# Optimization experiments

Measured on AMD Instinct MI355X. Metric: run time of the kernel, lower is better.

Reference implementation:

```python
import jax, jax.numpy as jnp
import numpy as np
from jax import lax

EPS = 1e-08
PAD = 1  # kernel_size // 2 for k=3


def setup_inputs() -> dict:
    key = jax.random.key(0)
    k1, k2, k3, k4 = jax.random.split(key, 4)
    B, Cin, Cout, H, W, K, S = 16, 256, 256, 64, 64, 3, 512
    x = jax.random.normal(k1, (B, Cin, H, W), dtype=jnp.float32)
    style = jax.random.normal(k2, (B, S), dtype=jnp.float32)
    mod_weight = jax.random.normal(k3, (Cin, S), dtype=jnp.float32)
    mod_bias = jnp.zeros((Cin,), dtype=jnp.float32)
    weight = jax.random.normal(k4, (1, Cout, Cin, K, K), dtype=jnp.float32)
    bias = jnp.zeros((1, Cout, 1, 1), dtype=jnp.float32)
    return {"x": x, "style": style, "mod_weight": mod_weight,
            "mod_bias": mod_bias, "weight": weight, "bias": bias}


def reference(x, style, mod_weight, mod_bias, weight, bias):
    # EqualizedLinear modulation (lr_mul = 1.0): s[b, cin]
    s = style @ mod_weight.T + mod_bias  # [B, Cin]
    # per-sample modulated weights: [B, Cout, Cin, K, K]
    w = weight * s[:, None, :, None, None]
    # demodulation: rsqrt of sum over (Cin, K, K)
    demod = lax.rsqrt(jnp.sum(w * w, axis=(2, 3, 4)) + EPS)  # [B, Cout]
    w = w * demod[:, :, None, None, None]

    # per-sample conv2d (groups=B equivalent) via vmap over batch
    def conv_one(xb, wb):
        # xb: [Cin, H, W], wb: [Cout, Cin, K, K]
        return lax.conv_general_dilated(
            xb[None], wb, window_strides=(1, 1),
            padding=[(PAD, PAD), (PAD, PAD)],
            dimension_numbers=("NCHW", "OIHW", "NCHW"))[0]

    out = jax.vmap(conv_one)(x, w)  # [B, Cout, H, W]
    return out + bias
```

## Files before the change

kernel.cpp:

```cpp
#include <hip/hip_runtime.h>

#define EPS 1e-8f
#define THREADS 512

typedef __attribute__((ext_vector_type(8))) short short8;
typedef __attribute__((ext_vector_type(4))) float f32x4;
typedef __attribute__((ext_vector_type(8))) unsigned short u16x8;

static __device__ __forceinline__ unsigned short f2bf(float f) {
  unsigned int u = __float_as_uint(f);
  u += 0x7FFF + ((u >> 16) & 1);
  return (unsigned short)(u >> 16);
}

__global__ void k_prep(const float* __restrict__ style, const float* __restrict__ mw,
                       const float* __restrict__ mb, float* __restrict__ s_out,
                       const float* __restrict__ weight, float* __restrict__ wsq,
                       unsigned short* __restrict__ wbf) {
  __shared__ float sm[2304];
  int t = threadIdx.x;
  if (blockIdx.x < 16) {
    int b = blockIdx.x;
    sm[t]       = style[b*512 + t];
    sm[t + 256] = style[b*512 + 256 + t];
    __syncthreads();
    const float4* row = (const float4*)(mw + (size_t)t*512);
    float acc = 0.f;
#pragma unroll 4
    for (int i = 0; i < 128; ++i) {
      float4 m = row[i];
      acc += m.x*sm[4*i] + m.y*sm[4*i+1] + m.z*sm[4*i+2] + m.w*sm[4*i+3];
    }
    s_out[b*256 + t] = acc + mb[t];
  } else {
    int co = blockIdx.x - 16;
    for (int q = t; q < 576; q += 256)
      *(float4*)&sm[q*4] = *(const float4*)(weight + (size_t)co*2304 + q*4);
    __syncthreads();
    int ci = t;
    int c = ci >> 6, cil = ci & 63;
    int base = ((co*128 + cil*2) ^ ((co & 7) << 4)) >> 1;
    float sum = 0.f;
#pragma unroll
    for (int r = 0; r < 9; ++r) {
      float v = sm[ci*9 + r];
      sum += v*v;
      wbf[(size_t)(c*9 + r)*16384 + base] = f2bf(v);
    }
    wsq[co*256 + ci] = sum;
  }
}

__global__ void k_demod(const float* __restrict__ s, const float* __restrict__ wsq,
                        float* __restrict__ dm) {
  int b = blockIdx.x, t = threadIdx.x;
  __shared__ float s2[256];
  float sv = s[b*256 + t];
  s2[t] = sv*sv;
  __syncthreads();
  const float4* row = (const float4*)(wsq + (size_t)t*256);
  float acc = 0.f;
#pragma unroll 4
  for (int i = 0; i < 64; ++i) {
    float4 q = row[i];
    acc += q.x*s2[4*i] + q.y*s2[4*i+1] + q.z*s2[4*i+2] + q.w*s2[4*i+3];
  }
  dm[b*256 + t] = rsqrtf(acc + EPS);
}

__global__ void k_pad(const float* __restrict__ x, const float* __restrict__ s,
                      unsigned short* __restrict__ xp) {
  int bid = blockIdx.x;
  int b = bid / 66, gh = bid - b*66;
  int t = threadIdx.x;
  size_t rowbase = (size_t)(b*66 + gh) * (66*256);
  u16x8* rp = (u16x8*)(xp + rowbase);
  if (gh == 0 || gh == 65) {
    u16x8 z = (u16x8)0;
    for (int q = t; q < 2112; q += 256) rp[q] = z;
    return;
  }
  int h = gh - 1;
  __shared__ float sl[256];
  __shared__ unsigned short xl[64*256];
  sl[t] = s[b*256 + t];
  __syncthreads();
  int w4 = (t & 15) * 4, o0 = t >> 4;
#pragma unroll
  for (int p = 0; p < 2; ++p) {
    int oct = o0 + p*16;
    u16x8 outv[4];
#pragma unroll
    for (int j = 0; j < 8; ++j) {
      int ci = oct*8 + j;
      float4 v = *(const float4*)(x + ((size_t)(b*256 + ci)*64 + h)*64 + w4);
      float sc = sl[ci];
      outv[0][j] = (short)f2bf(v.x * sc);
      outv[1][j] = (short)f2bf(v.y * sc);
      outv[2][j] = (short)f2bf(v.z * sc);
      outv[3][j] = (short)f2bf(v.w * sc);
    }
#pragma unroll
    for (int k = 0; k < 4; ++k) {
      int w = w4 + k;
      int byte = w*512 + ((oct ^ (w & 31)) << 4);
      *(u16x8*)((char*)xl + byte) = outv[k];
    }
  }
  __syncthreads();
  u16x8 z = (u16x8)0;
  if (t < 32) rp[t] = z;
  else if (t < 64) rp[65*32 + (t - 32)] = z;
  for (int q = t; q < 2048; q += 256) {
    int w2 = q >> 5, slot = q & 31;
    u16x8 v = *(const u16x8*)((char*)xl + w2*512 + ((slot ^ (w2 & 31)) << 4));
    rp[(w2 + 1)*32 + slot] = v;
  }
}

__global__ __launch_bounds__(512, 2)
void k_conv(const unsigned short* __restrict__ xp, const unsigned short* __restrict__ wbf,
            const float* __restrict__ dm, const float* __restrict__ bias,
            float* __restrict__ out) {
  __shared__ unsigned short x_lds[6*66*64];
  __shared__ unsigned short w_lds[2][256*64];

  const int tid = threadIdx.x;
  const int lane = tid & 63;
  const int wave = tid >> 6;
  const int b = blockIdx.x >> 4;
  const int h0 = (blockIdx.x & 15) * 4;
  const int wm = wave >> 1, wn = wave & 1;
  const int l15 = lane & 15, lk = lane >> 4;

  f32x4 acc[4][8];
#pragma unroll
  for (int m = 0; m < 4; ++m)
#pragma unroll
    for (int f = 0; f < 8; ++f) acc[m][f] = (f32x4)0.f;

  auto stage_x = [&](int c) {
    int cb = c*64;
#pragma unroll
    for (int it = 0; it < 7; ++it) {
      int q = it*THREADS + tid;
      if (q < 3168) {
        int hw = q >> 3;
        int hl = hw / 66, w = hw - hl*66;
        int slot = (q & 7) ^ (hw & 7);
        const unsigned short* src =
            xp + (size_t)((b*66 + h0 + hl)*66 + w)*256 + cb + slot*8;
        __builtin_amdgcn_global_load_lds(
            (const __attribute__((address_space(1))) void*)src,
            (__attribute__((address_space(3))) void*)&x_lds[(size_t)q*8],
            16, 0, 0);
      }
    }
  };
  auto stage_w = [&](int p, int buf) {
    const unsigned short* wsrc = wbf + (size_t)p*16384;
#pragma unroll
    for (int it = 0; it < 4; ++it) {
      int q = it*THREADS + tid;
      __builtin_amdgcn_global_load_lds(
          (const __attribute__((address_space(1))) void*)(wsrc + (size_t)q*8),
          (__attribute__((address_space(3))) void*)&w_lds[buf][(size_t)q*8],
          16, 0, 0);
    }
  };

  stage_x(0);
  stage_w(0, 0);
  __syncthreads();

  for (int c = 0; c < 4; ++c) {
    for (int r = 0; r < 9; ++r) {
      int p = c*9 + r;
      if (p < 35) stage_w(p + 1, (p + 1) & 1);
      const unsigned short* wb = w_lds[p & 1];
      int dh = r / 3, dw = r - dh*3;
#pragma unroll
      for (int kh = 0; kh < 2; ++kh) {
        int cio = kh*64 + lk*16;
        short8 a[4], bf[8];
#pragma unroll
        for (int m = 0; m < 4; ++m) {
          int co = wm*64 + m*16 + l15;
          int byte = (co*128 + cio) ^ ((co & 7) << 4);
          a[m] = *(const short8*)((const char*)wb + byte);
        }
#pragma unroll
        for (int f = 0; f < 8; ++f) {
          int row = (wn*2 + (f >> 2) + dh)*66 + ((f & 3)*16 + l15 + dw);
          int byte = (row*128 + cio) ^ ((row & 7) << 4);
          bf[f] = *(const short8*)((const char*)x_lds + byte);
        }
        __builtin_amdgcn_s_setprio(1);
#pragma unroll
        for (int m = 0; m < 4; ++m)
#pragma unroll
          for (int f = 0; f < 8; ++f)
            acc[m][f] = __builtin_amdgcn_mfma_f32_16x16x32_bf16(a[m], bf[f], acc[m][f], 0, 0, 0);
        __builtin_amdgcn_s_setprio(0);
      }
      if (r == 8) {
        __syncthreads();
        if (c < 3) stage_x(c + 1);
        __syncthreads();
      } else {
        __syncthreads();
      }
    }
  }

  int colane = (lane >> 4) * 4;
#pragma unroll
  for (int m = 0; m < 4; ++m) {
    int cob = wm*64 + m*16 + colane;
    float4 d4 = *(const float4*)&dm[b*256 + cob];
    float4 b4 = *(const float4*)&bias[cob];
#pragma unroll
    for (int f = 0; f < 8; ++f) {
      int h = h0 + wn*2 + (f >> 2);
      int wc = (f & 3)*16 + l15;
      float* op = out + ((size_t)(b*256 + cob)*64 + h)*64 + wc;
      op[0]     = acc[m][f][0] * d4.x + b4.x;
      op[4096]  = acc[m][f][1] * d4.y + b4.y;
      op[8192]  = acc[m][f][2] * d4.z + b4.z;
      op[12288] = acc[m][f][3] * d4.w + b4.w;
    }
  }
}

extern "C" void kernel_launch(void* const* d_in, const int* in_sizes, int n_in,
                              void* d_out, int out_size, void* d_ws, size_t ws_size,
                              hipStream_t stream) {
  const float* x      = (const float*)d_in[0];
  const float* style  = (const float*)d_in[1];
  const float* mw     = (const float*)d_in[2];
  const float* mb     = (const float*)d_in[3];
  const float* weight = (const float*)d_in[4];
  const float* bias   = (const float*)d_in[5];
  float* out = (float*)d_out;

  char* ws = (char*)d_ws;
  float* s_buf        = (float*)(ws);
  float* wsq          = (float*)(ws + 16384);
  float* dmod         = (float*)(ws + 16384 + 262144);
  unsigned short* wbf = (unsigned short*)(ws + 294912);
  unsigned short* xpd = (unsigned short*)(ws + 294912 + 1179648);

  k_prep<<<272, 256, 0, stream>>>(style, mw, mb, s_buf, weight, wsq, wbf);
  k_demod<<<16, 256, 0, stream>>>(s_buf, wsq, dmod);
  k_pad<<<16*66, 256, 0, stream>>>(x, s_buf, xpd);
  k_conv<<<256, 512, 0, stream>>>(xpd, wbf, dmod, bias, out);
}
```

Before: 224.3 us.

## Fuse demodulation into conv kernel and pipeline x staging with explicit waitcnts

Removes the separate demod kernel and computes per-sample demodulation factors inside the conv kernel prologue, overlapping with the initial LDS staging. Replaces __syncthreads with explicit vmcnt waits and raw barriers so x tiles for the next channel chunk are issued together with weight prefetches. Saves a launch and some barrier overhead, at the cost of redundant demod work per block (16 blocks per batch recompute it) and more delicate synchronization.

```diff
diff --git a/kernel.cpp b/kernel.cpp
--- a/kernel.cpp
+++ b/kernel.cpp
@@ -51,23 +51,6 @@
   }
 }
 
-__global__ void k_demod(const float* __restrict__ s, const float* __restrict__ wsq,
-                        float* __restrict__ dm) {
-  int b = blockIdx.x, t = threadIdx.x;
-  __shared__ float s2[256];
-  float sv = s[b*256 + t];
-  s2[t] = sv*sv;
-  __syncthreads();
-  const float4* row = (const float4*)(wsq + (size_t)t*256);
-  float acc = 0.f;
-#pragma unroll 4
-  for (int i = 0; i < 64; ++i) {
-    float4 q = row[i];
-    acc += q.x*s2[4*i] + q.y*s2[4*i+1] + q.z*s2[4*i+2] + q.w*s2[4*i+3];
-  }
-  dm[b*256 + t] = rsqrtf(acc + EPS);
-}
-
 __global__ void k_pad(const float* __restrict__ x, const float* __restrict__ s,
                       unsigned short* __restrict__ xp) {
   int bid = blockIdx.x;
@@ -120,10 +103,12 @@
 
 __global__ __launch_bounds__(512, 2)
 void k_conv(const unsigned short* __restrict__ xp, const unsigned short* __restrict__ wbf,
-            const float* __restrict__ dm, const float* __restrict__ bias,
-            float* __restrict__ out) {
-  __shared__ unsigned short x_lds[6*66*64];
-  __shared__ unsigned short w_lds[2][256*64];
+            const float* __restrict__ s_buf, const float* __restrict__ wsq,
+            const float* __restrict__ bias, float* __restrict__ out) {
+  __shared__ unsigned short x_lds[3168*8];
+  __shared__ unsigned short w_lds[2*16384];
+  __shared__ float s2s[256];
+  __shared__ float dms[256];
 
   const int tid = threadIdx.x;
   const int lane = tid & 63;
@@ -132,12 +117,6 @@
   const int h0 = (blockIdx.x & 15) * 4;
   const int wm = wave >> 1, wn = wave & 1;
   const int l15 = lane & 15, lk = lane >> 4;
-
-  f32x4 acc[4][8];
-#pragma unroll
-  for (int m = 0; m < 4; ++m)
-#pragma unroll
-    for (int f = 0; f < 8; ++f) acc[m][f] = (f32x4)0.f;
 
   auto stage_x = [&](int c) {
     int cb = c*64;
@@ -157,59 +136,89 @@
       }
     }
   };
-  auto stage_w = [&](int p, int buf) {
+  auto stage_w = [&](int p) {
     const unsigned short* wsrc = wbf + (size_t)p*16384;
+    unsigned short* dst = &w_lds[(p & 1)*16384];
 #pragma unroll
     for (int it = 0; it < 4; ++it) {
       int q = it*THREADS + tid;
       __builtin_amdgcn_global_load_lds(
           (const __attribute__((address_space(1))) void*)(wsrc + (size_t)q*8),
-          (__attribute__((address_space(3))) void*)&w_lds[buf][(size_t)q*8],
+          (__attribute__((address_space(3))) void*)&dst[(size_t)q*8],
           16, 0, 0);
     }
   };
 
   stage_x(0);
-  stage_w(0, 0);
-  __syncthreads();
+  stage_w(0);
+
+  if (tid < 256) { float sv = s_buf[b*256 + tid]; s2s[tid] = sv*sv; }
+  asm volatile("s_waitcnt lgkmcnt(0)" ::: "memory");
+  __builtin_amdgcn_s_barrier();
+  {
+    int co = tid >> 1, half = tid & 1;
+    const float4* row = (const float4*)(wsq + (size_t)co*256 + half*128);
+    const float* sp = &s2s[half*128];
+    float a = 0.f;
+#pragma unroll 4
+    for (int i = 0; i < 32; ++i) {
+      float4 q = row[i];
+      a += q.x*sp[4*i] + q.y*sp[4*i+1] + q.z*sp[4*i+2] + q.w*sp[4*i+3];
+    }
+    a += __shfl_xor(a, 1);
+    if (half == 0) dms[co] = rsqrtf(a + EPS);
+  }
+
+  f32x4 acc[4][8];
+#pragma unroll
+  for (int m = 0; m < 4; ++m)
+#pragma unroll
+    for (int f = 0; f < 8; ++f) acc[m][f] = (f32x4)0.f;
+
+  asm volatile("s_waitcnt vmcnt(0) lgkmcnt(0)" ::: "memory");
+  __builtin_amdgcn_s_barrier();
 
   for (int c = 0; c < 4; ++c) {
     for (int r = 0; r < 9; ++r) {
       int p = c*9 + r;
-      if (p < 35) stage_w(p + 1, (p + 1) & 1);
-      const unsigned short* wb = w_lds[p & 1];
+      if (r == 0 && c > 0) stage_x(c);
+      if (p < 35) {
+        stage_w(p + 1);
+        asm volatile("s_waitcnt vmcnt(4)" ::: "memory");
+      } else {
+        asm volatile("s_waitcnt vmcnt(0)" ::: "memory");
+      }
+      __builtin_amdgcn_s_barrier();
+      __builtin_amdgcn_sched_barrier(0);
+
+      const unsigned short* wbp = &w_lds[(p & 1)*16384];
       int dh = r / 3, dw = r - dh*3;
 #pragma unroll
       for (int kh = 0; kh < 2; ++kh) {
         int cio = kh*64 + lk*16;
-        short8 a[4], bf[8];
+        short8 a[4], bv[8];
 #pragma unroll
         for (int m = 0; m < 4; ++m) {
           int co = wm*64 + m*16 + l15;
           int byte = (co*128 + cio) ^ ((co & 7) << 4);
-          a[m] = *(const short8*)((const char*)wb + byte);
+          a[m] = *(const short8*)((const char*)wbp + byte);
         }
 #pragma unroll
         for (int f = 0; f < 8; ++f) {
           int row = (wn*2 + (f >> 2) + dh)*66 + ((f & 3)*16 + l15 + dw);
           int byte = (row*128 + cio) ^ ((row & 7) << 4);
-          bf[f] = *(const short8*)((const char*)x_lds + byte);
+          bv[f] = *(const short8*)((const char*)x_lds + byte);
         }
         __builtin_amdgcn_s_setprio(1);
 #pragma unroll
         for (int m = 0; m < 4; ++m)
 #pragma unroll
           for (int f = 0; f < 8; ++f)
-            acc[m][f] = __builtin_amdgcn_mfma_f32_16x16x32_bf16(a[m], bf[f], acc[m][f], 0, 0, 0);
+            acc[m][f] = __builtin_amdgcn_mfma_f32_16x16x32_bf16(a[m], bv[f], acc[m][f], 0, 0, 0);
         __builtin_amdgcn_s_setprio(0);
       }
-      if (r == 8) {
-        __syncthreads();
-        if (c < 3) stage_x(c + 1);
-        __syncthreads();
-      } else {
-        __syncthreads();
-      }
+      __builtin_amdgcn_sched_barrier(0);
+      __builtin_amdgcn_s_barrier();
     }
   }
 
@@ -217,7 +226,7 @@
 #pragma unroll
   for (int m = 0; m < 4; ++m) {
     int cob = wm*64 + m*16 + colane;
-    float4 d4 = *(const float4*)&dm[b*256 + cob];
+    float4 d4 = *(const float4*)&dms[cob];
     float4 b4 = *(const float4*)&bias[cob];
 #pragma unroll
     for (int f = 0; f < 8; ++f) {
@@ -246,12 +255,10 @@
   char* ws = (char*)d_ws;
   float* s_buf        = (float*)(ws);
   float* wsq          = (float*)(ws + 16384);
-  float* dmod         = (float*)(ws + 16384 + 262144);
   unsigned short* wbf = (unsigned short*)(ws + 294912);
   unsigned short* xpd = (unsigned short*)(ws + 294912 + 1179648);
 
   k_prep<<<272, 256, 0, stream>>>(style, mw, mb, s_buf, weight, wsq, wbf);
-  k_demod<<<16, 256, 0, stream>>>(s_buf, wsq, dmod);
   k_pad<<<16*66, 256, 0, stream>>>(x, s_buf, xpd);
-  k_conv<<<256, 512, 0, stream>>>(xpd, wbf, dmod, bias, out);
-}
+  k_conv<<<256, 512, 0, stream>>>(xpd, wbf, s_buf, wsq, bias, out);
+}
```

New measurement: 218.0 us. 2.8% less time.
